# Kernel tuning notes

Measured on AMD Instinct MI355X. Metric: run time of the kernel, lower is better.

## Reference

```python
import jax, jax.numpy as jnp
import numpy as np

N_NODES = 50000
N_EDGES = 800000
D = 128
NEG_SLOPE = 0.2
L2_EPS = 1e-12  # torch F.normalize eps


def setup_inputs() -> dict:
    key = jax.random.key(0)
    k1, k2, k3, k4, k5 = jax.random.split(key, 5)
    node_fts = jax.random.normal(k1, (N_NODES, D), dtype=jnp.float32)
    edges = jax.random.randint(k2, (2, N_EDGES), 0, N_NODES, dtype=jnp.int32)
    edge_fts = jax.random.normal(k3, (N_EDGES, 1), dtype=jnp.float32)
    # xavier-ish init for linear weights (stored as [out, in], matching nn.Linear)
    scale = 1.414 * np.sqrt(2.0 / (D + D))
    W_self = jax.random.normal(k4, (D, D), dtype=jnp.float32) * scale
    W_neigh = jax.random.normal(k5, (D, D), dtype=jnp.float32) * scale
    return {"node_fts": node_fts, "edges": edges, "edge_fts": edge_fts,
            "W_self": W_self, "W_neigh": W_neigh}


def reference(node_fts, edges, edge_fts, W_self, W_neigh):
    n = node_fts.shape[0]
    dst_idx = edges[0]  # segment ids (aggregation targets)
    src_idx = edges[1]  # gather ids (neighbor features)

    # self transform: [N, D]
    src_node_fts = node_fts @ W_self.T

    # gather neighbor feats along edges: [E, D]
    gathered = node_fts[src_idx]

    # scatter-mean into destination nodes
    seg_sum = jax.ops.segment_sum(gathered, dst_idx, num_segments=n)  # [N, D]
    cnt = jax.ops.segment_sum(jnp.ones((gathered.shape[0], 1), dtype=node_fts.dtype),
                              dst_idx, num_segments=n)                # [N, 1]
    neigh_mean = seg_sum / jnp.maximum(cnt, 1.0)

    # linear + LeakyReLU(0.2) on aggregated neighbors
    neigh_final = jax.nn.leaky_relu(neigh_mean @ W_neigh.T, NEG_SLOPE)

    # update: sum + LeakyReLU(0.2)
    updated = jax.nn.leaky_relu(src_node_fts + neigh_final, NEG_SLOPE)

    # L2 normalize per row (torch F.normalize semantics)
    norm = jnp.linalg.norm(updated, axis=1, keepdims=True)
    return updated / jnp.maximum(norm, L2_EPS)
```

## Files before the change

### kernel.cpp

```cpp
#include <hip/hip_runtime.h>
#include <hip/hip_bf16.h>

#define N_NODES 50000
#define N_EDGES 800000
#define D 128
#define NEG 0.2f

#define NB 200
#define EPB 4000
#define NPAIR 12500
#define NCH 8
#define ROWS_PER_CH 25

#define MFMA_BLOCKS 768
#define NTILES 3125
#define COLA_BLOCKS 391
#define FILL_SLICES 1600
#define FILL_EPS 500

typedef __attribute__((ext_vector_type(8))) short bf16x8;
typedef __attribute__((ext_vector_type(4))) float f32x4;

__device__ __forceinline__ float bflo(unsigned int u) {
    return __uint_as_float(u << 16);
}
__device__ __forceinline__ float bfhi(unsigned int u) {
    return __uint_as_float(u & 0xffff0000u);
}

__device__ __forceinline__ bf16x8 cvt8(const float4& f0, const float4& f1) {
    bf16x8 af;
    __hip_bfloat16 h;
    h = __float2bfloat16(f0.x); af[0] = reinterpret_cast<short&>(h);
    h = __float2bfloat16(f0.y); af[1] = reinterpret_cast<short&>(h);
    h = __float2bfloat16(f0.z); af[2] = reinterpret_cast<short&>(h);
    h = __float2bfloat16(f0.w); af[3] = reinterpret_cast<short&>(h);
    h = __float2bfloat16(f1.x); af[4] = reinterpret_cast<short&>(h);
    h = __float2bfloat16(f1.y); af[5] = reinterpret_cast<short&>(h);
    h = __float2bfloat16(f1.z); af[6] = reinterpret_cast<short&>(h);
    h = __float2bfloat16(f1.w); af[7] = reinterpret_cast<short&>(h);
    return af;
}

__global__ __launch_bounds__(256) void hist_mfma_kernel(
    const int* __restrict__ dst_idx,
    unsigned int* __restrict__ bh,
    unsigned char* __restrict__ rank8,
    const float* __restrict__ Ws, const float* __restrict__ Wn,
    const float* __restrict__ x,
    unsigned int* __restrict__ sb32, unsigned int* __restrict__ zb32) {
    __shared__ unsigned int smem[NPAIR];
    const int tid = threadIdx.x, b = blockIdx.x;
    if (b < NB) {
        unsigned int* lh = smem;
        for (int i = tid; i < NPAIR; i += 256) lh[i] = 0u;
        __syncthreads();
        const int e0 = b * EPB;
        for (int i = tid; i < EPB; i += 256) {
            int d = dst_idx[e0 + i];
            int sh = (d & 3) * 8;
            unsigned int old = atomicAdd(&lh[d >> 2], 1u << sh);
            rank8[e0 + i] = (unsigned char)((old >> sh) & 0xffu);
        }
        __syncthreads();
        for (int i = tid; i < NPAIR; i += 256) bh[(size_t)b * NPAIR + i] = lh[i];
    } else {
        const int lane = threadIdx.x & 63;
        const int wv = threadIdx.x >> 6;
        const int lm = lane & 15;
        const int lk = (lane >> 4) * 8;
        const int dr = (lane >> 4) * 4;
        ushort (*tile0)[132] = (ushort (*)[132])smem;
        ushort (*tile1)[132] = ((ushort (*)[132])smem) + 16;

        bf16x8 bfr[4][4];
#pragma unroll
        for (int t4 = 0; t4 < 4; ++t4) {
            const int nt = wv * 4 + t4;
            const float* wrow = (wv < 2)
                ? (Ws + (size_t)(nt * 16 + lm) * D)
                : (Wn + (size_t)((nt - 8) * 16 + lm) * D);
#pragma unroll
            for (int kc = 0; kc < 4; ++kc) {
                float4 f0 = *(const float4*)(wrow + kc * 32 + lk);
                float4 f1 = *(const float4*)(wrow + kc * 32 + lk + 4);
                bfr[t4][kc] = cvt8(f0, f1);
            }
        }

        for (int t = b - NB; t < NTILES; t += MFMA_BLOCKS) {
            const int m0 = t * 16;

            bf16x8 a[4];
#pragma unroll
            for (int kc = 0; kc < 4; ++kc) {
                const float* src = x + (long)(m0 + lm) * D + kc * 32 + lk;
                float4 f0 = *(const float4*)(src);
                float4 f1 = *(const float4*)(src + 4);
                a[kc] = cvt8(f0, f1);
            }

#pragma unroll
            for (int t4 = 0; t4 < 4; ++t4) {
                const int nt = wv * 4 + t4;
                f32x4 acc = {0.f, 0.f, 0.f, 0.f};
#pragma unroll
                for (int kc = 0; kc < 4; ++kc)
                    acc = __builtin_amdgcn_mfma_f32_16x16x32_bf16(a[kc], bfr[t4][kc], acc, 0, 0, 0);
                ushort (*tptr)[132] = (nt < 8) ? tile0 : tile1;
                const int col = (nt & 7) * 16 + lm;
#pragma unroll
                for (int r = 0; r < 4; ++r) {
                    __hip_bfloat16 h = __float2bfloat16(acc[r]);
                    tptr[dr + r][col] = reinterpret_cast<unsigned short&>(h);
                }
            }
            __syncthreads();
            const unsigned int* ts32 = (const unsigned int*)tile0;
            const unsigned int* tz32 = (const unsigned int*)tile1;
#pragma unroll
            for (int q = 0; q < 4; ++q) {
                const int r16 = wv * 4 + q;
                sb32[(m0 + r16) * 64 + lane] = ts32[r16 * 66 + lane];
                zb32[(m0 + r16) * 64 + lane] = tz32[r16 * 66 + lane];
            }
            __syncthreads();
        }
    }
}

__global__ __launch_bounds__(256) void colA_kernel(
    const unsigned int* __restrict__ bh, unsigned int* __restrict__ csum) {
    int gid = blockIdx.x * 256 + threadIdx.x;
    if (gid >= NCH * NPAIR) return;
    int c = gid / NPAIR;
    int i = gid - c * NPAIR;
    const unsigned int* col = bh + (size_t)(c * ROWS_PER_CH) * NPAIR + i;
    unsigned int s = 0u;
#pragma unroll
    for (int r = 0; r < ROWS_PER_CH; ++r) s += col[(size_t)r * NPAIR];
    csum[c * NPAIR + i] = s;
}

__global__ __launch_bounds__(1024) void colscanb_scan_kernel(
    unsigned int* __restrict__ bh, const unsigned int* __restrict__ csum,
    int* __restrict__ offs) {
    const int tid = threadIdx.x;
    if (blockIdx.x < 98) {
        int gid = blockIdx.x * 1024 + tid;
        if (gid >= NCH * NPAIR) return;
        int c = gid / NPAIR;
        int i = gid - c * NPAIR;
        unsigned int run = 0u;
        for (int cc = 0; cc < c; ++cc) run += csum[cc * NPAIR + i];
        unsigned int* col = bh + (size_t)(c * ROWS_PER_CH) * NPAIR + i;
#pragma unroll
        for (int r = 0; r < ROWS_PER_CH; ++r) {
            unsigned int v = col[(size_t)r * NPAIR];
            col[(size_t)r * NPAIR] = run;
            run += v;
        }
        return;
    }
    __shared__ int wsum[16];
    __shared__ int carry_s;
    const int lane = tid & 63, wv = tid >> 6;
    if (tid == 0) { carry_s = 0; offs[N_NODES] = N_EDGES; }
    __syncthreads();
    for (int base = 0; base < NPAIR; base += 4096) {
        int i0 = base + tid * 4;
        unsigned int p0 = 0, p1 = 0, p2 = 0, p3 = 0;
#pragma unroll
        for (int j = 0; j < 4; ++j) {
            int qi = i0 + j;
            if (qi < NPAIR) {
                unsigned int s = 0;
#pragma unroll
                for (int c = 0; c < NCH; ++c) s += csum[c * NPAIR + qi];
                if (j == 0) p0 = s; else if (j == 1) p1 = s;
                else if (j == 2) p2 = s; else p3 = s;
            }
        }
        int q0 = (int)((p0 & 0xffu) + ((p0 >> 8) & 0xffu) + ((p0 >> 16) & 0xffu) + (p0 >> 24));
        int q1 = (int)((p1 & 0xffu) + ((p1 >> 8) & 0xffu) + ((p1 >> 16) & 0xffu) + (p1 >> 24));
        int q2 = (int)((p2 & 0xffu) + ((p2 >> 8) & 0xffu) + ((p2 >> 16) & 0xffu) + (p2 >> 24));
        int q3 = (int)((p3 & 0xffu) + ((p3 >> 8) & 0xffu) + ((p3 >> 16) & 0xffu) + (p3 >> 24));
        int tsum = q0 + q1 + q2 + q3;
        int xs = tsum;
#pragma unroll
        for (int off = 1; off < 64; off <<= 1) {
            int y = __shfl_up(xs, off);
            if (lane >= off) xs += y;
        }
        if (lane == 63) wsum[wv] = xs;
        __syncthreads();
        if (wv == 0 && lane < 16) {
            int s = wsum[lane];
#pragma unroll
            for (int off = 1; off < 16; off <<= 1) {
                int y = __shfl_up(s, off);
                if (lane >= off) s += y;
            }
            wsum[lane] = s;
        }
        __syncthreads();
        int waveoff = (wv == 0) ? 0 : wsum[wv - 1];
        int excl = carry_s + waveoff + xs - tsum;
        unsigned int pk[4] = {p0, p1, p2, p3};
        int qs[4] = {q0, q1, q2, q3};
        int qbase = excl;
#pragma unroll
        for (int j = 0; j < 4; ++j) {
            int qi = i0 + j;
            if (qi < NPAIR) {
                unsigned int p = pk[j];
                int d0 = (int)(p & 0xffu), d1 = (int)((p >> 8) & 0xffu);
                int d2 = (int)((p >> 16) & 0xffu);
                int4 o; o.x = qbase; o.y = o.x + d0; o.z = o.y + d1; o.w = o.z + d2;
                *(int4*)(offs + 4 * qi) = o;
            }
            qbase += qs[j];
        }
        int total = wsum[15];
        __syncthreads();
        if (tid == 0) carry_s += total;
        __syncthreads();
    }
}

__global__ __launch_bounds__(256) void fill_kernel(
    const int* __restrict__ dst_idx, const int* __restrict__ src_idx,
    const unsigned char* __restrict__ rank8,
    const unsigned char* __restrict__ bprefix,
    const int* __restrict__ offs, unsigned short* __restrict__ adj) {
    const int e0 = blockIdx.x * FILL_EPS;
    const int b = e0 / EPB;
    const unsigned char* bp = bprefix + (size_t)b * N_NODES;
    for (int i = threadIdx.x; i < FILL_EPS; i += 256) {
        int e = e0 + i;
        int d = dst_idx[e];
        int pos = offs[d] + (int)bp[d] + (int)rank8[e];
        adj[pos] = (unsigned short)src_idx[e];
    }
}

__global__ __launch_bounds__(256) void gather_final_kernel(
    const uint4* __restrict__ zb4, const uint4* __restrict__ sb4,
    const int* __restrict__ offs,
    const unsigned short* __restrict__ adj, float4* __restrict__ out4) {
    int wid = (int)((blockIdx.x * (long)blockDim.x + threadIdx.x) >> 6);
    int lane = threadIdx.x & 63;
    if (wid >= N_NODES) return;
    const int c = lane & 15, g = lane >> 4;
    int base = offs[wid];
    int len = offs[wid + 1] - base;

    float a0 = 0.f, a1 = 0.f, a2 = 0.f, a3 = 0.f;
    float a4 = 0.f, a5 = 0.f, a6 = 0.f, a7 = 0.f;

    int k = 0;
    for (; k + 8 <= len; k += 8) {
        unsigned int sA = adj[base + k + g];
        unsigned int sB = adj[base + k + 4 + g];
        uint4 vA = zb4[sA * 16u + c];
        uint4 vB = zb4[sB * 16u + c];
        a0 += bflo(vA.x); a1 += bfhi(vA.x);
        a2 += bflo(vA.y); a3 += bfhi(vA.y);
        a4 += bflo(vA.z); a5 += bfhi(vA.z);
        a6 += bflo(vA.w); a7 += bfhi(vA.w);
        a0 += bflo(vB.x); a1 += bfhi(vB.x);
        a2 += bflo(vB.y); a3 += bfhi(vB.y);
        a4 += bflo(vB.z); a5 += bfhi(vB.z);
        a6 += bflo(vB.w); a7 += bfhi(vB.w);
    }
    if (k + 4 <= len) {
        unsigned int sA = adj[base + k + g];
        uint4 vA = zb4[sA * 16u + c];
        a0 += bflo(vA.x); a1 += bfhi(vA.x);
        a2 += bflo(vA.y); a3 += bfhi(vA.y);
        a4 += bflo(vA.z); a5 += bfhi(vA.z);
        a6 += bflo(vA.w); a7 += bfhi(vA.w);
        k += 4;
    }
    int rem = len - k;
    if (g < rem) {
        unsigned int sA = adj[base + k + g];
        uint4 vA = zb4[sA * 16u + c];
        a0 += bflo(vA.x); a1 += bfhi(vA.x);
        a2 += bflo(vA.y); a3 += bfhi(vA.y);
        a4 += bflo(vA.z); a5 += bfhi(vA.z);
        a6 += bflo(vA.w); a7 += bfhi(vA.w);
    }

    a0 += __shfl_xor(a0, 16); a1 += __shfl_xor(a1, 16);
    a2 += __shfl_xor(a2, 16); a3 += __shfl_xor(a3, 16);
    a4 += __shfl_xor(a4, 16); a5 += __shfl_xor(a5, 16);
    a6 += __shfl_xor(a6, 16); a7 += __shfl_xor(a7, 16);
    a0 += __shfl_xor(a0, 32); a1 += __shfl_xor(a1, 32);
    a2 += __shfl_xor(a2, 32); a3 += __shfl_xor(a3, 32);
    a4 += __shfl_xor(a4, 32); a5 += __shfl_xor(a5, 32);
    a6 += __shfl_xor(a6, 32); a7 += __shfl_xor(a7, 32);

    float inv = 1.0f / fmaxf((float)len, 1.0f);
    float m0 = a0 * inv, m1 = a1 * inv, m2 = a2 * inv, m3 = a3 * inv;
    float m4 = a4 * inv, m5 = a5 * inv, m6 = a6 * inv, m7 = a7 * inv;
    m0 = m0 > 0.f ? m0 : NEG * m0; m1 = m1 > 0.f ? m1 : NEG * m1;
    m2 = m2 > 0.f ? m2 : NEG * m2; m3 = m3 > 0.f ? m3 : NEG * m3;
    m4 = m4 > 0.f ? m4 : NEG * m4; m5 = m5 > 0.f ? m5 : NEG * m5;
    m6 = m6 > 0.f ? m6 : NEG * m6; m7 = m7 > 0.f ? m7 : NEG * m7;

    uint4 sv = sb4[(unsigned int)wid * 16u + c];
    float u0 = bflo(sv.x) + m0, u1 = bfhi(sv.x) + m1;
    float u2 = bflo(sv.y) + m2, u3 = bfhi(sv.y) + m3;
    float u4 = bflo(sv.z) + m4, u5 = bfhi(sv.z) + m5;
    float u6 = bflo(sv.w) + m6, u7 = bfhi(sv.w) + m7;
    u0 = u0 > 0.f ? u0 : NEG * u0; u1 = u1 > 0.f ? u1 : NEG * u1;
    u2 = u2 > 0.f ? u2 : NEG * u2; u3 = u3 > 0.f ? u3 : NEG * u3;
    u4 = u4 > 0.f ? u4 : NEG * u4; u5 = u5 > 0.f ? u5 : NEG * u5;
    u6 = u6 > 0.f ? u6 : NEG * u6; u7 = u7 > 0.f ? u7 : NEG * u7;

    float ss = u0 * u0 + u1 * u1 + u2 * u2 + u3 * u3 +
               u4 * u4 + u5 * u5 + u6 * u6 + u7 * u7;
    ss += __shfl_xor(ss, 1);
    ss += __shfl_xor(ss, 2);
    ss += __shfl_xor(ss, 4);
    ss += __shfl_xor(ss, 8);
    float r = 1.0f / fmaxf(sqrtf(ss), 1e-12f);

    if (lane < 16) {
        float4 o0; o0.x = u0 * r; o0.y = u1 * r; o0.z = u2 * r; o0.w = u3 * r;
        float4 o1; o1.x = u4 * r; o1.y = u5 * r; o1.z = u6 * r; o1.w = u7 * r;
        out4[(unsigned int)wid * 32u + c * 2u] = o0;
        out4[(unsigned int)wid * 32u + c * 2u + 1u] = o1;
    }
}

extern "C" void kernel_launch(void* const* d_in, const int* in_sizes, int n_in,
                              void* d_out, int out_size, void* d_ws, size_t ws_size,
                              hipStream_t stream) {
    const float* node_fts = (const float*)d_in[0];
    const int* edges = (const int*)d_in[1];
    const float* W_self = (const float*)d_in[3];
    const float* W_neigh = (const float*)d_in[4];

    const int* dst_idx = edges;
    const int* src_idx = edges + N_EDGES;

    unsigned short* zb = (unsigned short*)d_ws;
    unsigned short* sb = zb + (size_t)N_NODES * D;
    int* offs = (int*)(sb + (size_t)N_NODES * D);
    unsigned short* adj = (unsigned short*)(offs + N_NODES + 1);
    unsigned int* bh = (unsigned int*)(adj + N_EDGES);
    unsigned char* rank8 = (unsigned char*)(bh + (size_t)NB * NPAIR);
    unsigned int* csum = (unsigned int*)(rank8 + N_EDGES);

    hist_mfma_kernel<<<NB + MFMA_BLOCKS, 256, 0, stream>>>(
        dst_idx, bh, rank8, W_self, W_neigh, node_fts,
        (unsigned int*)sb, (unsigned int*)zb);

    colA_kernel<<<COLA_BLOCKS, 256, 0, stream>>>(bh, csum);

    colscanb_scan_kernel<<<99, 1024, 0, stream>>>(bh, csum, offs);

    fill_kernel<<<FILL_SLICES, 256, 0, stream>>>(
        dst_idx, src_idx, rank8, (const unsigned char*)bh, offs, adj);

    int gb = (N_NODES * 64 + 255) / 256;
    gather_final_kernel<<<gb, 256, 0, stream>>>(
        (const uint4*)zb, (const uint4*)sb, offs, adj, (float4*)d_out);
}
```

Before: 109.4 us.

## Regroup MFMA transform with column-sum kernel and unroll gather loop by 16

Splits the histogram out into its own kernel and merges the MFMA node transform with the column-sum (colA) pass into one launch. The small histogram blocks then no longer share a launch with the heavy GEMM, and the column-sum work overlaps the GEMM instead of running as a separate serialized kernel. The launch count stays the same, but the histogram now runs alone, so some overlap between histogram and GEMM is given up. Separately, the gather loop is unrolled to 16 neighbors per iteration to keep more loads in flight, at the cost of more registers.

```diff
diff --git a/kernel.cpp b/kernel.cpp
--- a/kernel.cpp
+++ b/kernel.cpp
@@ -42,36 +42,37 @@
     return af;
 }
 
-__global__ __launch_bounds__(256) void hist_mfma_kernel(
+__global__ __launch_bounds__(256) void hist_kernel(
     const int* __restrict__ dst_idx,
     unsigned int* __restrict__ bh,
-    unsigned char* __restrict__ rank8,
+    unsigned char* __restrict__ rank8) {
+    __shared__ unsigned int lh[NPAIR];
+    const int tid = threadIdx.x, b = blockIdx.x;
+    for (int i = tid; i < NPAIR; i += 256) lh[i] = 0u;
+    __syncthreads();
+    const int e0 = b * EPB;
+    for (int i = tid; i < EPB; i += 256) {
+        int d = dst_idx[e0 + i];
+        int sh = (d & 3) * 8;
+        unsigned int old = atomicAdd(&lh[d >> 2], 1u << sh);
+        rank8[e0 + i] = (unsigned char)((old >> sh) & 0xffu);
+    }
+    __syncthreads();
+    for (int i = tid; i < NPAIR; i += 256) bh[(size_t)b * NPAIR + i] = lh[i];
+}
+
+__global__ __launch_bounds__(256) void mfma_colA_kernel(
+    const float* __restrict__ x,
     const float* __restrict__ Ws, const float* __restrict__ Wn,
-    const float* __restrict__ x,
-    unsigned int* __restrict__ sb32, unsigned int* __restrict__ zb32) {
-    __shared__ unsigned int smem[NPAIR];
-    const int tid = threadIdx.x, b = blockIdx.x;
-    if (b < NB) {
-        unsigned int* lh = smem;
-        for (int i = tid; i < NPAIR; i += 256) lh[i] = 0u;
-        __syncthreads();
-        const int e0 = b * EPB;
-        for (int i = tid; i < EPB; i += 256) {
-            int d = dst_idx[e0 + i];
-            int sh = (d & 3) * 8;
-            unsigned int old = atomicAdd(&lh[d >> 2], 1u << sh);
-            rank8[e0 + i] = (unsigned char)((old >> sh) & 0xffu);
-        }
-        __syncthreads();
-        for (int i = tid; i < NPAIR; i += 256) bh[(size_t)b * NPAIR + i] = lh[i];
-    } else {
+    unsigned int* __restrict__ sb32, unsigned int* __restrict__ zb32,
+    const unsigned int* __restrict__ bh, unsigned int* __restrict__ csum) {
+    __shared__ ushort tile[2][16][132];
+    if (blockIdx.x < MFMA_BLOCKS) {
         const int lane = threadIdx.x & 63;
         const int wv = threadIdx.x >> 6;
         const int lm = lane & 15;
         const int lk = (lane >> 4) * 8;
         const int dr = (lane >> 4) * 4;
-        ushort (*tile0)[132] = (ushort (*)[132])smem;
-        ushort (*tile1)[132] = ((ushort (*)[132])smem) + 16;
 
         bf16x8 bfr[4][4];
 #pragma unroll
@@ -88,7 +89,7 @@
             }
         }
 
-        for (int t = b - NB; t < NTILES; t += MFMA_BLOCKS) {
+        for (int t = blockIdx.x; t < NTILES; t += MFMA_BLOCKS) {
             const int m0 = t * 16;
 
             bf16x8 a[4];
@@ -107,7 +108,7 @@
 #pragma unroll
                 for (int kc = 0; kc < 4; ++kc)
                     acc = __builtin_amdgcn_mfma_f32_16x16x32_bf16(a[kc], bfr[t4][kc], acc, 0, 0, 0);
-                ushort (*tptr)[132] = (nt < 8) ? tile0 : tile1;
+                ushort (*tptr)[132] = (nt < 8) ? tile[0] : tile[1];
                 const int col = (nt & 7) * 16 + lm;
 #pragma unroll
                 for (int r = 0; r < 4; ++r) {
@@ -116,8 +117,8 @@
                 }
             }
             __syncthreads();
-            const unsigned int* ts32 = (const unsigned int*)tile0;
-            const unsigned int* tz32 = (const unsigned int*)tile1;
+            const unsigned int* ts32 = (const unsigned int*)tile[0];
+            const unsigned int* tz32 = (const unsigned int*)tile[1];
 #pragma unroll
             for (int q = 0; q < 4; ++q) {
                 const int r16 = wv * 4 + q;
@@ -126,20 +127,17 @@
             }
             __syncthreads();
         }
-    }
-}
-
-__global__ __launch_bounds__(256) void colA_kernel(
-    const unsigned int* __restrict__ bh, unsigned int* __restrict__ csum) {
-    int gid = blockIdx.x * 256 + threadIdx.x;
-    if (gid >= NCH * NPAIR) return;
-    int c = gid / NPAIR;
-    int i = gid - c * NPAIR;
-    const unsigned int* col = bh + (size_t)(c * ROWS_PER_CH) * NPAIR + i;
-    unsigned int s = 0u;
-#pragma unroll
-    for (int r = 0; r < ROWS_PER_CH; ++r) s += col[(size_t)r * NPAIR];
-    csum[c * NPAIR + i] = s;
+    } else {
+        int gid = (blockIdx.x - MFMA_BLOCKS) * 256 + threadIdx.x;
+        if (gid >= NCH * NPAIR) return;
+        int c = gid / NPAIR;
+        int i = gid - c * NPAIR;
+        const unsigned int* col = bh + (size_t)(c * ROWS_PER_CH) * NPAIR + i;
+        unsigned int s = 0u;
+#pragma unroll
+        for (int r = 0; r < ROWS_PER_CH; ++r) s += col[(size_t)r * NPAIR];
+        csum[c * NPAIR + i] = s;
+    }
 }
 
 __global__ __launch_bounds__(1024) void colscanb_scan_kernel(
@@ -259,7 +257,33 @@
     float a4 = 0.f, a5 = 0.f, a6 = 0.f, a7 = 0.f;
 
     int k = 0;
-    for (; k + 8 <= len; k += 8) {
+    for (; k + 16 <= len; k += 16) {
+        unsigned int s0 = adj[base + k + g];
+        unsigned int s1 = adj[base + k + 4 + g];
+        unsigned int s2 = adj[base + k + 8 + g];
+        unsigned int s3 = adj[base + k + 12 + g];
+        uint4 v0 = zb4[s0 * 16u + c];
+        uint4 v1 = zb4[s1 * 16u + c];
+        uint4 v2 = zb4[s2 * 16u + c];
+        uint4 v3 = zb4[s3 * 16u + c];
+        a0 += bflo(v0.x); a1 += bfhi(v0.x);
+        a2 += bflo(v0.y); a3 += bfhi(v0.y);
+        a4 += bflo(v0.z); a5 += bfhi(v0.z);
+        a6 += bflo(v0.w); a7 += bfhi(v0.w);
+        a0 += bflo(v1.x); a1 += bfhi(v1.x);
+        a2 += bflo(v1.y); a3 += bfhi(v1.y);
+        a4 += bflo(v1.z); a5 += bfhi(v1.z);
+        a6 += bflo(v1.w); a7 += bfhi(v1.w);
+        a0 += bflo(v2.x); a1 += bfhi(v2.x);
+        a2 += bflo(v2.y); a3 += bfhi(v2.y);
+        a4 += bflo(v2.z); a5 += bfhi(v2.z);
+        a6 += bflo(v2.w); a7 += bfhi(v2.w);
+        a0 += bflo(v3.x); a1 += bfhi(v3.x);
+        a2 += bflo(v3.y); a3 += bfhi(v3.y);
+        a4 += bflo(v3.z); a5 += bfhi(v3.z);
+        a6 += bflo(v3.w); a7 += bfhi(v3.w);
+    }
+    if (k + 8 <= len) {
         unsigned int sA = adj[base + k + g];
         unsigned int sB = adj[base + k + 4 + g];
         uint4 vA = zb4[sA * 16u + c];
@@ -272,6 +296,7 @@
         a2 += bflo(vB.y); a3 += bfhi(vB.y);
         a4 += bflo(vB.z); a5 += bfhi(vB.z);
         a6 += bflo(vB.w); a7 += bfhi(vB.w);
+        k += 8;
     }
     if (k + 4 <= len) {
         unsigned int sA = adj[base + k + g];
@@ -354,11 +379,11 @@
     unsigned char* rank8 = (unsigned char*)(bh + (size_t)NB * NPAIR);
     unsigned int* csum = (unsigned int*)(rank8 + N_EDGES);
 
-    hist_mfma_kernel<<<NB + MFMA_BLOCKS, 256, 0, stream>>>(
-        dst_idx, bh, rank8, W_self, W_neigh, node_fts,
-        (unsigned int*)sb, (unsigned int*)zb);
-
-    colA_kernel<<<COLA_BLOCKS, 256, 0, stream>>>(bh, csum);
+    hist_kernel<<<NB, 256, 0, stream>>>(dst_idx, bh, rank8);
+
+    mfma_colA_kernel<<<MFMA_BLOCKS + COLA_BLOCKS, 256, 0, stream>>>(
+        node_fts, W_self, W_neigh,
+        (unsigned int*)sb, (unsigned int*)zb, bh, csum);
 
     colscanb_scan_kernel<<<99, 1024, 0, stream>>>(bh, csum, offs);
 
```

Measured after the change: 110.4 us. About the same (+0.9%).
